# Optimization experiments

Hardware: AMD Instinct MI355X
Metric: run time of the kernel (lower is better)

The kernel has to match this reference:

```python
import jax, jax.numpy as jnp
import numpy as np

N_TOK = 131072
N_EMB = 1024
EMB_DIM = 64
COMMIT = 0.25


def setup_inputs() -> dict:
    key = jax.random.key(0)
    k1, k2 = jax.random.split(key)
    z_e = jax.random.normal(k1, (N_TOK, EMB_DIM), dtype=jnp.float32)
    # nn.init.uniform_(weight, -1/K, 1/K)
    codebook = jax.random.uniform(k2, (N_EMB, EMB_DIM), dtype=jnp.float32,
                                  minval=-1.0 / N_EMB, maxval=1.0 / N_EMB)
    return {"z_e": z_e, "codebook": codebook}


def reference(z_e, codebook):
    sg = jax.lax.stop_gradient
    # ||a-b||^2 = ||a||^2 + ||b||^2 - 2 a.b  (avoids [N,K,D] broadcast)
    d = (jnp.sum(z_e * z_e, axis=-1, keepdims=True)          # [N,1]
         + jnp.sum(codebook * codebook, axis=-1)[None, :]    # [1,K]
         - 2.0 * jnp.einsum('nd,kd->nk', z_e, codebook))     # [N,K]
    indices = jnp.argmin(d, axis=-1)                          # [N] int
    z_q = codebook[indices]                                   # [N,D] gather

    codebook_loss = jnp.mean((z_q - sg(z_e)) ** 2)
    commitment_loss = jnp.mean((z_e - sg(z_q)) ** 2)
    loss = codebook_loss + COMMIT * commitment_loss

    z_q_st = z_e + sg(z_q - z_e)                              # straight-through

    # avg_probs = one_hot(indices).mean(0) via scatter-add histogram
    counts = jnp.zeros((N_EMB,), dtype=jnp.float32).at[indices].add(1.0)
    avg_probs = counts / z_e.shape[0]
    perplexity = jnp.exp(-jnp.sum(avg_probs * jnp.log(avg_probs + 1e-10)))

    return z_q_st, loss, perplexity, indices
```

## Files before the change

kernel.cpp:

```cpp
#include <hip/hip_runtime.h>
#include <math.h>

#define NTOK 131072
#define NEMB 1024
#define DIM  64
#define OUT_LOSS (NTOK * DIM)
#define OUT_PERP (OUT_LOSS + 1)
#define OUT_IDX  (OUT_LOSS + 2)

#define EPS_FLAG 6e-5f

typedef short bf16x8 __attribute__((ext_vector_type(8)));
typedef float f32x4  __attribute__((ext_vector_type(4)));
typedef const __attribute__((address_space(1))) void* gas_t;
typedef __attribute__((address_space(3))) void* las_t;

__device__ __forceinline__ float sqb(float x) {
    float y = x * x;
    asm volatile("" : "+v"(y));
    return y;
}
#define NP_PAIRWISE_SQ64(GET, RES)                                     \
    do {                                                               \
        float r0 = sqb(GET(0)), r1 = sqb(GET(1)), r2 = sqb(GET(2)),    \
              r3 = sqb(GET(3)), r4 = sqb(GET(4)), r5 = sqb(GET(5)),    \
              r6 = sqb(GET(6)), r7 = sqb(GET(7));                      \
        _Pragma("unroll")                                              \
        for (int i = 8; i < 64; i += 8) {                              \
            r0 += sqb(GET(i + 0)); r1 += sqb(GET(i + 1));              \
            r2 += sqb(GET(i + 2)); r3 += sqb(GET(i + 3));              \
            r4 += sqb(GET(i + 4)); r5 += sqb(GET(i + 5));              \
            r6 += sqb(GET(i + 6)); r7 += sqb(GET(i + 7));              \
        }                                                              \
        RES = ((r0 + r1) + (r2 + r3)) + ((r4 + r5) + (r6 + r7));       \
    } while (0)

__device__ __forceinline__ unsigned short f2bf_rne(float x) {
    unsigned u = __float_as_uint(x);
    u += 0x7FFFu + ((u >> 16) & 1u);
    return (unsigned short)(u >> 16);
}
__device__ __forceinline__ float bf2f(unsigned short b) {
    return __uint_as_float(((unsigned)b) << 16);
}


__global__ void vq_prep(const float* __restrict__ cb, float* __restrict__ h,
                        unsigned short* __restrict__ ch, unsigned short* __restrict__ cl,
                        double* __restrict__ sse, int* __restrict__ counts,
                        int* __restrict__ done) {
    if (blockIdx.x == 0) {
        if (threadIdx.x == 0) { *sse = 0.0; *done = 0; }
        for (int i = threadIdx.x; i < NEMB * 16; i += 256) counts[i] = 0;
    }
    int k = blockIdx.x * 256 + threadIdx.x;
    if (k >= NEMB) return;
    float c[64];
    const float4* p = (const float4*)(cb + k * DIM);
#pragma unroll
    for (int q = 0; q < 16; ++q) {
        float4 v = p[q];
        c[4 * q] = v.x; c[4 * q + 1] = v.y; c[4 * q + 2] = v.z; c[4 * q + 3] = v.w;
    }
    float hk;
#define GETC(d) (c[d])
    NP_PAIRWISE_SQ64(GETC, hk);
#undef GETC
    h[k] = hk;
#pragma unroll
    for (int b = 0; b < 8; ++b) {
        unsigned uhv[4], ulv[4];
#pragma unroll
        for (int e = 0; e < 4; ++e) {
            float x0 = -2.0f * c[b * 8 + e * 2 + 0];
            float x1 = -2.0f * c[b * 8 + e * 2 + 1];
            unsigned short h0 = f2bf_rne(x0), h1 = f2bf_rne(x1);
            unsigned short l0 = f2bf_rne(x0 - bf2f(h0)), l1 = f2bf_rne(x1 - bf2f(h1));
            uhv[e] = (unsigned)h0 | ((unsigned)h1 << 16);
            ulv[e] = (unsigned)l0 | ((unsigned)l1 << 16);
        }
        *(uint4*)(ch + k * 64 + b * 8) = make_uint4(uhv[0], uhv[1], uhv[2], uhv[3]);
        *(uint4*)(cl + k * 64 + b * 8) = make_uint4(ulv[0], ulv[1], ulv[2], ulv[3]);
    }
}

__global__ __launch_bounds__(512) void vq_screen(
    const float*          __restrict__ ze,
    const float*          __restrict__ cb,
    const unsigned short* __restrict__ ch_g,
    const unsigned short* __restrict__ cl_g,
    const float*          __restrict__ h_g,
    float*                __restrict__ out,
    double*               __restrict__ sse_g,
    int*                  __restrict__ counts) {
    __shared__ __align__(16) char lds[53376];
    const int tid  = threadIdx.x;
    const int lane = tid & 63;
    const int wid  = tid >> 6;
    const int col  = lane & 15;
    const int grp  = lane >> 4;
    const int tbase = blockIdx.x * 256 + wid * 32;

    const int srow = tid >> 3, scol = tid & 7;
    const int srcoff = (srow * 8 + (scol ^ (srow & 7))) * 16;

    bf16x8 zh[2][2], zl[2][2];
#pragma unroll
    for (int tt = 0; tt < 2; ++tt)
#pragma unroll
        for (int s = 0; s < 2; ++s) {
            const float* zp = ze + (size_t)(tbase + tt * 16 + col) * 64 + s * 32 + grp * 8;
            float4 v0 = *(const float4*)(zp);
            float4 v1 = *(const float4*)(zp + 4);
            float zv[8] = {v0.x, v0.y, v0.z, v0.w, v1.x, v1.y, v1.z, v1.w};
            bf16x8 hfr, lfr;
#pragma unroll
            for (int j = 0; j < 8; ++j) {
                unsigned short hb = f2bf_rne(zv[j]);
                unsigned short lb = f2bf_rne(zv[j] - bf2f(hb));
                hfr[j] = (short)hb;
                lfr[j] = (short)lb;
            }
            zh[tt][s] = hfr;
            zl[tt][s] = lfr;
        }

    float m1[2] = {INFINITY, INFINITY}, m2[2] = {INFINITY, INFINITY};
    int   ki[2] = {0, 0};

#define STAGE(cc, b)                                                           \
    do {                                                                       \
        __builtin_amdgcn_global_load_lds(                                      \
            (gas_t)((const char*)ch_g + (cc) * 8192 + srcoff),                 \
            (las_t)(lds + (b) * 16384 + wid * 1024), 16, 0, 0);                \
        __builtin_amdgcn_global_load_lds(                                      \
            (gas_t)((const char*)cl_g + (cc) * 8192 + srcoff),                 \
            (las_t)(lds + (b) * 16384 + 8192 + wid * 1024), 16, 0, 0);         \
    } while (0)

#define COMPUTE(cc, b)                                                         \
    do {                                                                       \
        _Pragma("unroll")                                                      \
        for (int ct = 0; ct < 4; ++ct) {                                       \
            const int arow = (b) * 16384 + ct * 2048 + col * 128;              \
            bf16x8 ach0 = *(const bf16x8*)(lds + arow + ((((0 * 4) + grp) ^ (col & 7)) << 4)); \
            bf16x8 ach1 = *(const bf16x8*)(lds + arow + ((((1 * 4) + grp) ^ (col & 7)) << 4)); \
            bf16x8 acl0 = *(const bf16x8*)(lds + arow + 8192 + ((((0 * 4) + grp) ^ (col & 7)) << 4)); \
            bf16x8 acl1 = *(const bf16x8*)(lds + arow + 8192 + ((((1 * 4) + grp) ^ (col & 7)) << 4)); \
            f32x4 hv = *(const f32x4*)(lds + 49152 + (cc) * 256 + ct * 64 + grp * 16); \
            f32x4 acc0 = hv, acc1 = hv;                                        \
            acc0 = __builtin_amdgcn_mfma_f32_16x16x32_bf16(ach0, zh[0][0], acc0, 0, 0, 0); \
            acc1 = __builtin_amdgcn_mfma_f32_16x16x32_bf16(ach0, zh[1][0], acc1, 0, 0, 0); \
            acc0 = __builtin_amdgcn_mfma_f32_16x16x32_bf16(ach1, zh[0][1], acc0, 0, 0, 0); \
            acc1 = __builtin_amdgcn_mfma_f32_16x16x32_bf16(ach1, zh[1][1], acc1, 0, 0, 0); \
            acc0 = __builtin_amdgcn_mfma_f32_16x16x32_bf16(ach0, zl[0][0], acc0, 0, 0, 0); \
            acc1 = __builtin_amdgcn_mfma_f32_16x16x32_bf16(ach0, zl[1][0], acc1, 0, 0, 0); \
            acc0 = __builtin_amdgcn_mfma_f32_16x16x32_bf16(ach1, zl[0][1], acc0, 0, 0, 0); \
            acc1 = __builtin_amdgcn_mfma_f32_16x16x32_bf16(ach1, zl[1][1], acc1, 0, 0, 0); \
            acc0 = __builtin_amdgcn_mfma_f32_16x16x32_bf16(acl0, zh[0][0], acc0, 0, 0, 0); \
            acc1 = __builtin_amdgcn_mfma_f32_16x16x32_bf16(acl0, zh[1][0], acc1, 0, 0, 0); \
            acc0 = __builtin_amdgcn_mfma_f32_16x16x32_bf16(acl1, zh[0][1], acc0, 0, 0, 0); \
            acc1 = __builtin_amdgcn_mfma_f32_16x16x32_bf16(acl1, zh[1][1], acc1, 0, 0, 0); \
            const int kb = (cc) * 64 + ct * 16 + grp * 4;                      \
            _Pragma("unroll")                                                  \
            for (int j = 0; j < 4; ++j) {                                      \
                float s0 = acc0[j], s1 = acc1[j];                              \
                bool lt0 = s0 < m1[0], lt1 = s1 < m1[1];                       \
                m2[0] = fminf(m2[0], fmaxf(s0, m1[0]));                        \
                m2[1] = fminf(m2[1], fmaxf(s1, m1[1]));                        \
                ki[0] = lt0 ? (kb + j) : ki[0];                                \
                ki[1] = lt1 ? (kb + j) : ki[1];                                \
                m1[0] = fminf(m1[0], s0);                                      \
                m1[1] = fminf(m1[1], s1);                                      \
            }                                                                  \
        }                                                                      \
    } while (0)

#define CHUNK(cc, W)                                                           \
    do {                                                                       \
        asm volatile("s_waitcnt vmcnt(" #W ")" ::: "memory");                  \
        __builtin_amdgcn_s_barrier();                                          \
        __builtin_amdgcn_sched_barrier(0);                                     \
        if ((cc) + 2 < 16) STAGE((cc) + 2, ((cc) + 2) % 3);                    \
        COMPUTE(cc, (cc) % 3);                                                 \
    } while (0)

    __builtin_amdgcn_global_load_lds((gas_t)(h_g + tid),
                                     (las_t)(lds + 49152 + wid * 256), 4, 0, 0);
    __builtin_amdgcn_global_load_lds((gas_t)(h_g + 512 + tid),
                                     (las_t)(lds + 49152 + 2048 + wid * 256), 4, 0, 0);
    STAGE(0, 0);
    STAGE(1, 1);

    CHUNK(0, 2);  CHUNK(1, 2);  CHUNK(2, 2);  CHUNK(3, 2);
    CHUNK(4, 2);  CHUNK(5, 2);  CHUNK(6, 2);  CHUNK(7, 2);
    CHUNK(8, 2);  CHUNK(9, 2);  CHUNK(10, 2); CHUNK(11, 2);
    CHUNK(12, 2); CHUNK(13, 2); CHUNK(14, 2); CHUNK(15, 0);

#pragma unroll
    for (int d = 16; d <= 32; d <<= 1) {
#pragma unroll
        for (int tt = 0; tt < 2; ++tt) {
            float om1 = __shfl_xor(m1[tt], d, 64);
            float om2 = __shfl_xor(m2[tt], d, 64);
            int   oki = __shfl_xor(ki[tt], d, 64);
            m2[tt] = fminf(fminf(m2[tt], om2), fmaxf(m1[tt], om1));
            ki[tt] = (om1 < m1[tt]) ? oki : ki[tt];
            m1[tt] = fminf(m1[tt], om1);
        }
    }
    unsigned flagpack = ((m2[0] - m1[0] < EPS_FLAG) ? 1u : 0u)
                      | ((m2[1] - m1[1] < EPS_FLAG) ? 2u : 0u);
    if (lane < 16) {
#pragma unroll
        for (int tt = 0; tt < 2; ++tt) {
            int t = tbase + tt * 16 + lane;
            bool flag = (flagpack >> tt) & 1u;
            out[OUT_IDX + t] = flag ? -(float)(ki[tt] + 1) : (float)ki[tt];
        }
    }

    double lsse = 0.0;
    const int d4 = lane & 15;
#pragma unroll
    for (int iter = 0; iter < 8; ++iter) {
        const int j   = iter * 4 + grp;
        const int tt  = iter >> 2;
        const int src = j & 15;
        int k = __shfl(ki[tt], src, 64);
        unsigned fp = __shfl(flagpack, src, 64);
        if (!((fp >> tt) & 1u)) {
            const int t = tbase + j;
            float4 q  = *(const float4*)(cb + k * DIM + d4 * 4);
            float4 zv = *(const float4*)(ze + (size_t)t * DIM + d4 * 4);
            *(float4*)(out + (size_t)t * DIM + d4 * 4) = q;
            double dx = (double)q.x - (double)zv.x;
            double dy = (double)q.y - (double)zv.y;
            double dz = (double)q.z - (double)zv.z;
            double dw = (double)q.w - (double)zv.w;
            lsse = fma(dx, dx, lsse); lsse = fma(dy, dy, lsse);
            lsse = fma(dz, dz, lsse); lsse = fma(dw, dw, lsse);
            if (d4 == 0) atomicAdd(&counts[k * 16], 1);
        }
    }
#pragma unroll
    for (int off = 32; off > 0; off >>= 1)
        lsse += __shfl_down(lsse, off, 64);
    double* red = (double*)(lds + 53312);
    if (lane == 0) red[wid] = lsse;
    __syncthreads();
    if (tid == 0) {
        double bs = ((red[0] + red[1]) + (red[2] + red[3]))
                  + ((red[4] + red[5]) + (red[6] + red[7]));
        atomicAdd(sse_g, bs);
    }
}

__global__ __launch_bounds__(512) void vq_rescue(
    const float* __restrict__ ze, const float* __restrict__ cb,
    const float* __restrict__ h_g, float* __restrict__ out,
    double* __restrict__ sse_g, int* __restrict__ counts,
    int* __restrict__ done) {
    __shared__ __align__(16) float4 cbl[512 * 17];
    __shared__ float zst[8][64];
    __shared__ unsigned long long keys[8][64];
    __shared__ float hl[NEMB];
    __shared__ int loc[512];
    __shared__ int nloc;
    __shared__ double red[8];
    __shared__ int flagS;
    const int tid  = threadIdx.x;
    const int lane = tid & 63;
    const int wid  = tid >> 6;
    const int tbase = blockIdx.x * 512;

    if (tid == 0) nloc = 0;
    for (int i = tid; i < NEMB; i += 512) hl[i] = h_g[i];
    __syncthreads();
    float fidx = out[OUT_IDX + tbase + tid];
    if (fidx < 0.0f) { int s = atomicAdd(&nloc, 1); loc[s] = tid; }
    __syncthreads();
    const int nq = nloc;
    double lsse = 0.0;

    if (nq > 0) {
        const float4* cb4 = (const float4*)cb;
        for (int hf = 0; hf < 2; ++hf) {
            __syncthreads();
#pragma unroll
            for (int j = 0; j < 16; ++j) {
                int f = tid + j * 512;
                int code = f >> 4, d4 = f & 15;
                cbl[code * 17 + d4] = cb4[(size_t)(hf * 512 + code) * 16 + d4];
            }
            __syncthreads();

            for (int i = wid; i < nq; i += 8) {
                const int t = tbase + loc[i];
                const int slot = i >> 3;

                zst[wid][lane] = ze[(size_t)t * 64 + lane];
                __builtin_amdgcn_wave_barrier();
                asm volatile("s_waitcnt lgkmcnt(0)" ::: "memory");
                __builtin_amdgcn_sched_barrier(0);

                float sz;
#define GZ(d) (zst[wid][d])
                NP_PAIRWISE_SQ64(GZ, sz);
#undef GZ

                float acc[8] = {0.f, 0.f, 0.f, 0.f, 0.f, 0.f, 0.f, 0.f};
                const float4* zr4 = (const float4*)zst[wid];
#pragma unroll
                for (int d4 = 0; d4 < 16; ++d4) {
                    float4 zq = zr4[d4];
#pragma unroll
                    for (int cc = 0; cc < 8; ++cc) {
                        float4 cv = cbl[(lane + 64 * cc) * 17 + d4];
                        acc[cc] = fmaf(cv.x, zq.x, acc[cc]);
                        acc[cc] = fmaf(cv.y, zq.y, acc[cc]);
                        acc[cc] = fmaf(cv.z, zq.z, acc[cc]);
                        acc[cc] = fmaf(cv.w, zq.w, acc[cc]);
                    }
                }
                unsigned long long key = ~0ull;
#pragma unroll
                for (int cc = 0; cc < 8; ++cc) {
                    unsigned k = (unsigned)(hf * 512 + lane + 64 * cc);
                    float dk = (sz + hl[k]) - 2.0f * acc[cc];
                    unsigned long long c =
                        ((unsigned long long)__float_as_uint(dk) << 32) | k;
                    key = c < key ? c : key;
                }
#pragma unroll
                for (int dd = 1; dd < 64; dd <<= 1) {
                    unsigned long long o = __shfl_xor(key, dd, 64);
                    key = o < key ? o : key;
                }
                if (hf == 0) {
                    if (lane == 0) keys[wid][slot] = key;
                } else {
                    unsigned long long k0 = keys[wid][slot];
                    if (k0 < key) key = k0;
                    int newk = (int)(unsigned)(key & 0xFFFFFFFFull);
                    float q  = cb[newk * 64 + lane];
                    float zv = zst[wid][lane];
                    out[(size_t)t * 64 + lane] = q;
                    double diff = (double)q - (double)zv;
                    lsse = fma(diff, diff, lsse);
                    if (lane == 0) {
                        out[OUT_IDX + t] = (float)newk;
                        atomicAdd(&counts[newk * 16], 1);
                    }
                }
            }
        }
    }

#pragma unroll
    for (int off = 32; off > 0; off >>= 1)
        lsse += __shfl_down(lsse, off, 64);
    if (lane == 0) red[wid] = lsse;
    __syncthreads();
    if (tid == 0) {
        double bs = ((red[0] + red[1]) + (red[2] + red[3]))
                  + ((red[4] + red[5]) + (red[6] + red[7]));
        if (bs != 0.0) atomicAdd(sse_g, bs);
        __threadfence();
        flagS = (atomicAdd(done, 1) == 255);
    }
    __syncthreads();

    if (flagS) {
        __threadfence();
        double* red2 = (double*)cbl;
        double local = 0.0;
        for (int k = tid; k < NEMB; k += 512) {
            int cv = __hip_atomic_load(&counts[k * 16], __ATOMIC_RELAXED, __HIP_MEMORY_SCOPE_AGENT);
            double p = (double)cv / (double)NTOK;
            local += p * log(p + 1e-10);
        }
        red2[tid] = local;
        __syncthreads();
        for (int s = 256; s > 0; s >>= 1) {
            if (tid < s) red2[tid] += red2[tid + s];
            __syncthreads();
        }
        if (tid == 0) {
            double sv = __hip_atomic_load(sse_g, __ATOMIC_RELAXED, __HIP_MEMORY_SCOPE_AGENT);
            double mse = sv / ((double)NTOK * (double)DIM);
            out[OUT_LOSS] = (float)(1.25 * mse);
            out[OUT_PERP] = (float)exp(-red2[0]);
        }
    }
}

extern "C" void kernel_launch(void* const* d_in, const int* in_sizes, int n_in,
                              void* d_out, int out_size, void* d_ws, size_t ws_size,
                              hipStream_t stream) {
    const float* ze = (const float*)d_in[0];
    const float* cb = (const float*)d_in[1];
    float* out = (float*)d_out;

    char* w = (char*)d_ws;
    double*         sse    = (double*)w;
    int*            counts = (int*)(w + 64);
    int*            done   = (int*)(w + 65600);
    float*          h      = (float*)(w + 65664);
    unsigned short* ch     = (unsigned short*)(w + 69760);
    unsigned short* cl     = (unsigned short*)(w + 200832);

    vq_prep<<<NEMB / 256, 256, 0, stream>>>(cb, h, ch, cl, sse, counts, done);
    vq_screen<<<NTOK / 256, 512, 0, stream>>>(ze, cb, ch, cl, h, out, sse, counts);
    vq_rescue<<<NTOK / 512, 512, 0, stream>>>(ze, cb, h, out, sse, counts, done);
}
```

Before: 125.6 us.

## Double tokens per wave in screen kernel to amortize codebook LDS reads

Each wave now handles 64 tokens (four 16-token tiles) instead of 32, so every codebook fragment read from LDS feeds twice as many MFMAs. The grid is halved and the block keeps 512 threads. The MFMA chain is also restructured per tile into one dependent accumulator chain of six MFMAs. The tt index in the epilogue changes from iter>>2 to j>>4, which is equivalent to the old mapping. This raises register pressure (more z fragments and min state), adds a launch_bounds min-blocks hint, and reduces the number of blocks to 256, which may underfill the GPU. Each 6-MFMA chain per tile is serial, which may expose MFMA latency.

Result: slower. 157.0 us (+25.0%).

```diff
diff --git a/kernel.cpp b/kernel.cpp
--- a/kernel.cpp
+++ b/kernel.cpp
@@ -84,7 +84,7 @@
     }
 }
 
-__global__ __launch_bounds__(512) void vq_screen(
+__global__ __launch_bounds__(512, 4) void vq_screen(
     const float*          __restrict__ ze,
     const float*          __restrict__ cb,
     const unsigned short* __restrict__ ch_g,
@@ -99,14 +99,14 @@
     const int wid  = tid >> 6;
     const int col  = lane & 15;
     const int grp  = lane >> 4;
-    const int tbase = blockIdx.x * 256 + wid * 32;
+    const int tbase = blockIdx.x * 512 + wid * 64;
 
     const int srow = tid >> 3, scol = tid & 7;
     const int srcoff = (srow * 8 + (scol ^ (srow & 7))) * 16;
 
-    bf16x8 zh[2][2], zl[2][2];
-#pragma unroll
-    for (int tt = 0; tt < 2; ++tt)
+    bf16x8 zh[4][2], zl[4][2];
+#pragma unroll
+    for (int tt = 0; tt < 4; ++tt)
 #pragma unroll
         for (int s = 0; s < 2; ++s) {
             const float* zp = ze + (size_t)(tbase + tt * 16 + col) * 64 + s * 32 + grp * 8;
@@ -125,8 +125,9 @@
             zl[tt][s] = lfr;
         }
 
-    float m1[2] = {INFINITY, INFINITY}, m2[2] = {INFINITY, INFINITY};
-    int   ki[2] = {0, 0};
+    float m1[4] = {INFINITY, INFINITY, INFINITY, INFINITY};
+    float m2[4] = {INFINITY, INFINITY, INFINITY, INFINITY};
+    int   ki[4] = {0, 0, 0, 0};
 
 #define STAGE(cc, b)                                                           \
     do {                                                                       \
@@ -148,30 +149,23 @@
             bf16x8 acl0 = *(const bf16x8*)(lds + arow + 8192 + ((((0 * 4) + grp) ^ (col & 7)) << 4)); \
             bf16x8 acl1 = *(const bf16x8*)(lds + arow + 8192 + ((((1 * 4) + grp) ^ (col & 7)) << 4)); \
             f32x4 hv = *(const f32x4*)(lds + 49152 + (cc) * 256 + ct * 64 + grp * 16); \
-            f32x4 acc0 = hv, acc1 = hv;                                        \
-            acc0 = __builtin_amdgcn_mfma_f32_16x16x32_bf16(ach0, zh[0][0], acc0, 0, 0, 0); \
-            acc1 = __builtin_amdgcn_mfma_f32_16x16x32_bf16(ach0, zh[1][0], acc1, 0, 0, 0); \
-            acc0 = __builtin_amdgcn_mfma_f32_16x16x32_bf16(ach1, zh[0][1], acc0, 0, 0, 0); \
-            acc1 = __builtin_amdgcn_mfma_f32_16x16x32_bf16(ach1, zh[1][1], acc1, 0, 0, 0); \
-            acc0 = __builtin_amdgcn_mfma_f32_16x16x32_bf16(ach0, zl[0][0], acc0, 0, 0, 0); \
-            acc1 = __builtin_amdgcn_mfma_f32_16x16x32_bf16(ach0, zl[1][0], acc1, 0, 0, 0); \
-            acc0 = __builtin_amdgcn_mfma_f32_16x16x32_bf16(ach1, zl[0][1], acc0, 0, 0, 0); \
-            acc1 = __builtin_amdgcn_mfma_f32_16x16x32_bf16(ach1, zl[1][1], acc1, 0, 0, 0); \
-            acc0 = __builtin_amdgcn_mfma_f32_16x16x32_bf16(acl0, zh[0][0], acc0, 0, 0, 0); \
-            acc1 = __builtin_amdgcn_mfma_f32_16x16x32_bf16(acl0, zh[1][0], acc1, 0, 0, 0); \
-            acc0 = __builtin_amdgcn_mfma_f32_16x16x32_bf16(acl1, zh[0][1], acc0, 0, 0, 0); \
-            acc1 = __builtin_amdgcn_mfma_f32_16x16x32_bf16(acl1, zh[1][1], acc1, 0, 0, 0); \
             const int kb = (cc) * 64 + ct * 16 + grp * 4;                      \
             _Pragma("unroll")                                                  \
-            for (int j = 0; j < 4; ++j) {                                      \
-                float s0 = acc0[j], s1 = acc1[j];                              \
-                bool lt0 = s0 < m1[0], lt1 = s1 < m1[1];                       \
-                m2[0] = fminf(m2[0], fmaxf(s0, m1[0]));                        \
-                m2[1] = fminf(m2[1], fmaxf(s1, m1[1]));                        \
-                ki[0] = lt0 ? (kb + j) : ki[0];                                \
-                ki[1] = lt1 ? (kb + j) : ki[1];                                \
-                m1[0] = fminf(m1[0], s0);                                      \
-                m1[1] = fminf(m1[1], s1);                                      \
+            for (int tt = 0; tt < 4; ++tt) {                                   \
+                f32x4 acc = hv;                                                \
+                acc = __builtin_amdgcn_mfma_f32_16x16x32_bf16(ach0, zh[tt][0], acc, 0, 0, 0); \
+                acc = __builtin_amdgcn_mfma_f32_16x16x32_bf16(ach1, zh[tt][1], acc, 0, 0, 0); \
+                acc = __builtin_amdgcn_mfma_f32_16x16x32_bf16(ach0, zl[tt][0], acc, 0, 0, 0); \
+                acc = __builtin_amdgcn_mfma_f32_16x16x32_bf16(ach1, zl[tt][1], acc, 0, 0, 0); \
+                acc = __builtin_amdgcn_mfma_f32_16x16x32_bf16(acl0, zh[tt][0], acc, 0, 0, 0); \
+                acc = __builtin_amdgcn_mfma_f32_16x16x32_bf16(acl1, zh[tt][1], acc, 0, 0, 0); \
+                _Pragma("unroll")                                              \
+                for (int j = 0; j < 4; ++j) {                                  \
+                    float s = acc[j];                                          \
+                    m2[tt] = fminf(m2[tt], fmaxf(s, m1[tt]));                  \
+                    ki[tt] = (s < m1[tt]) ? (kb + j) : ki[tt];                 \
+                    m1[tt] = fminf(m1[tt], s);                                 \
+                }                                                              \
             }                                                                  \
         }                                                                      \
     } while (0)
@@ -200,7 +194,7 @@
 #pragma unroll
     for (int d = 16; d <= 32; d <<= 1) {
 #pragma unroll
-        for (int tt = 0; tt < 2; ++tt) {
+        for (int tt = 0; tt < 4; ++tt) {
             float om1 = __shfl_xor(m1[tt], d, 64);
             float om2 = __shfl_xor(m2[tt], d, 64);
             int   oki = __shfl_xor(ki[tt], d, 64);
@@ -210,10 +204,12 @@
         }
     }
     unsigned flagpack = ((m2[0] - m1[0] < EPS_FLAG) ? 1u : 0u)
-                      | ((m2[1] - m1[1] < EPS_FLAG) ? 2u : 0u);
+                      | ((m2[1] - m1[1] < EPS_FLAG) ? 2u : 0u)
+                      | ((m2[2] - m1[2] < EPS_FLAG) ? 4u : 0u)
+                      | ((m2[3] - m1[3] < EPS_FLAG) ? 8u : 0u);
     if (lane < 16) {
 #pragma unroll
-        for (int tt = 0; tt < 2; ++tt) {
+        for (int tt = 0; tt < 4; ++tt) {
             int t = tbase + tt * 16 + lane;
             bool flag = (flagpack >> tt) & 1u;
             out[OUT_IDX + t] = flag ? -(float)(ki[tt] + 1) : (float)ki[tt];
@@ -223,9 +219,9 @@
     double lsse = 0.0;
     const int d4 = lane & 15;
 #pragma unroll
-    for (int iter = 0; iter < 8; ++iter) {
+    for (int iter = 0; iter < 16; ++iter) {
         const int j   = iter * 4 + grp;
-        const int tt  = iter >> 2;
+        const int tt  = j >> 4;
         const int src = j & 15;
         int k = __shfl(ki[tt], src, 64);
         unsigned fp = __shfl(flagpack, src, 64);
@@ -411,6 +407,6 @@
     unsigned short* cl     = (unsigned short*)(w + 200832);
 
     vq_prep<<<NEMB / 256, 256, 0, stream>>>(cb, h, ch, cl, sse, counts, done);
-    vq_screen<<<NTOK / 256, 512, 0, stream>>>(ze, cb, ch, cl, h, out, sse, counts);
+    vq_screen<<<NTOK / 512, 512, 0, stream>>>(ze, cb, ch, cl, h, out, sse, counts);
     vq_rescue<<<NTOK / 512, 512, 0, stream>>>(ze, cb, h, out, sse, counts, done);
 }
```

## Track top-3 candidates in screen so rescue checks only two codes

Applied to the files above, without the earlier changes.

The screening kernel now keeps the best three distances per token instead of two. For flagged near-tie tokens it writes the runner-up index to an aux buffer, plus a bit saying whether the third candidate is also within the tie margin. The rescue kernel then does exact fp32 distances only against the top two codes for most flagged tokens, falling back to a full 1024-code scan only for 'deep' ties. This removes the large shared-memory codebook staging and full scans in rescue, at the cost of more compare/select work in the screen's hot loop and a correctness reliance on the third-best bound.

Measured after the change: 133.7 us. 1.06x slower.

```diff
diff --git a/kernel.cpp b/kernel.cpp
--- a/kernel.cpp
+++ b/kernel.cpp
@@ -91,6 +91,7 @@
     const unsigned short* __restrict__ cl_g,
     const float*          __restrict__ h_g,
     float*                __restrict__ out,
+    int*                  __restrict__ aux,
     double*               __restrict__ sse_g,
     int*                  __restrict__ counts) {
     __shared__ __align__(16) char lds[53376];
@@ -126,7 +127,8 @@
         }
 
     float m1[2] = {INFINITY, INFINITY}, m2[2] = {INFINITY, INFINITY};
-    int   ki[2] = {0, 0};
+    float m3[2] = {INFINITY, INFINITY};
+    int   ki[2] = {0, 0}, i2[2] = {0, 0};
 
 #define STAGE(cc, b)                                                           \
     do {                                                                       \
@@ -136,6 +138,16 @@
         __builtin_amdgcn_global_load_lds(                                      \
             (gas_t)((const char*)cl_g + (cc) * 8192 + srcoff),                 \
             (las_t)(lds + (b) * 16384 + 8192 + wid * 1024), 16, 0, 0);         \
+    } while (0)
+
+#define TOP3UPD(tt, s, kk)                                                     \
+    do {                                                                       \
+        bool lt1 = (s) < m1[tt], lt2 = (s) < m2[tt], lt3 = (s) < m3[tt];       \
+        m3[tt] = lt2 ? m2[tt] : (lt3 ? (s) : m3[tt]);                          \
+        i2[tt] = lt1 ? ki[tt] : (lt2 ? (kk) : i2[tt]);                         \
+        m2[tt] = lt1 ? m1[tt] : (lt2 ? (s) : m2[tt]);                          \
+        ki[tt] = lt1 ? (kk) : ki[tt];                                          \
+        m1[tt] = lt1 ? (s) : m1[tt];                                           \
     } while (0)
 
 #define COMPUTE(cc, b)                                                         \
@@ -164,14 +176,8 @@
             const int kb = (cc) * 64 + ct * 16 + grp * 4;                      \
             _Pragma("unroll")                                                  \
             for (int j = 0; j < 4; ++j) {                                      \
-                float s0 = acc0[j], s1 = acc1[j];                              \
-                bool lt0 = s0 < m1[0], lt1 = s1 < m1[1];                       \
-                m2[0] = fminf(m2[0], fmaxf(s0, m1[0]));                        \
-                m2[1] = fminf(m2[1], fmaxf(s1, m1[1]));                        \
-                ki[0] = lt0 ? (kb + j) : ki[0];                                \
-                ki[1] = lt1 ? (kb + j) : ki[1];                                \
-                m1[0] = fminf(m1[0], s0);                                      \
-                m1[1] = fminf(m1[1], s1);                                      \
+                TOP3UPD(0, acc0[j], kb + j);                                   \
+                TOP3UPD(1, acc1[j], kb + j);                                   \
             }                                                                  \
         }                                                                      \
     } while (0)
@@ -201,22 +207,42 @@
     for (int d = 16; d <= 32; d <<= 1) {
 #pragma unroll
         for (int tt = 0; tt < 2; ++tt) {
-            float om1 = __shfl_xor(m1[tt], d, 64);
-            float om2 = __shfl_xor(m2[tt], d, 64);
-            int   oki = __shfl_xor(ki[tt], d, 64);
-            m2[tt] = fminf(fminf(m2[tt], om2), fmaxf(m1[tt], om1));
-            ki[tt] = (om1 < m1[tt]) ? oki : ki[tt];
-            m1[tt] = fminf(m1[tt], om1);
+            float b1 = __shfl_xor(m1[tt], d, 64);
+            float b2 = __shfl_xor(m2[tt], d, 64);
+            float b3 = __shfl_xor(m3[tt], d, 64);
+            int  jb1 = __shfl_xor(ki[tt], d, 64);
+            int  jb2 = __shfl_xor(i2[tt], d, 64);
+            bool sw  = b1 < m1[tt];
+            float hi = sw ? m1[tt] : b1;
+            int  jhi = sw ? ki[tt] : jb1;
+            float c1 = sw ? b1 : m1[tt];
+            int   j1 = sw ? jb1 : ki[tt];
+            float mn2 = fminf(m2[tt], b2);
+            int   jm2 = (m2[tt] <= b2) ? i2[tt] : jb2;
+            float c2  = fminf(hi, mn2);
+            int   j2  = (hi <= mn2) ? jhi : jm2;
+            float mid = fmaxf(fminf(hi, m2[tt]),
+                              fminf(fmaxf(hi, m2[tt]), b2));
+            float c3  = fminf(mid, fminf(m3[tt], b3));
+            m1[tt] = c1; ki[tt] = j1; m2[tt] = c2; i2[tt] = j2; m3[tt] = c3;
         }
     }
     unsigned flagpack = ((m2[0] - m1[0] < EPS_FLAG) ? 1u : 0u)
                       | ((m2[1] - m1[1] < EPS_FLAG) ? 2u : 0u);
+    unsigned deeppack = ((m3[0] - m1[0] < EPS_FLAG) ? 1u : 0u)
+                      | ((m3[1] - m1[1] < EPS_FLAG) ? 2u : 0u);
     if (lane < 16) {
 #pragma unroll
         for (int tt = 0; tt < 2; ++tt) {
             int t = tbase + tt * 16 + lane;
             bool flag = (flagpack >> tt) & 1u;
-            out[OUT_IDX + t] = flag ? -(float)(ki[tt] + 1) : (float)ki[tt];
+            if (flag) {
+                out[OUT_IDX + t] = -(float)(ki[tt] + 1);
+                aux[t] = (int)((unsigned)i2[tt]
+                               | (((deeppack >> tt) & 1u) << 31));
+            } else {
+                out[OUT_IDX + t] = (float)ki[tt];
+            }
         }
     }
 
@@ -258,101 +284,123 @@
 
 __global__ __launch_bounds__(512) void vq_rescue(
     const float* __restrict__ ze, const float* __restrict__ cb,
-    const float* __restrict__ h_g, float* __restrict__ out,
-    double* __restrict__ sse_g, int* __restrict__ counts,
-    int* __restrict__ done) {
-    __shared__ __align__(16) float4 cbl[512 * 17];
+    const float* __restrict__ h_g, const int* __restrict__ aux,
+    float* __restrict__ out, double* __restrict__ sse_g,
+    int* __restrict__ counts, int* __restrict__ done) {
+    __shared__ int loc[512];
+    __shared__ int kfin[512];
+    __shared__ int dlist[512];
+    __shared__ int nloc, ndeep;
     __shared__ float zst[8][64];
-    __shared__ unsigned long long keys[8][64];
-    __shared__ float hl[NEMB];
-    __shared__ int loc[512];
-    __shared__ int nloc;
-    __shared__ double red[8];
+    __shared__ double red2[512];
     __shared__ int flagS;
     const int tid  = threadIdx.x;
     const int lane = tid & 63;
     const int wid  = tid >> 6;
     const int tbase = blockIdx.x * 512;
 
-    if (tid == 0) nloc = 0;
-    for (int i = tid; i < NEMB; i += 512) hl[i] = h_g[i];
+    if (tid == 0) { nloc = 0; ndeep = 0; }
     __syncthreads();
-    float fidx = out[OUT_IDX + tbase + tid];
-    if (fidx < 0.0f) { int s = atomicAdd(&nloc, 1); loc[s] = tid; }
+    {
+        float fidx = out[OUT_IDX + tbase + tid];
+        if (fidx < 0.0f) { int s = atomicAdd(&nloc, 1); loc[s] = tid; }
+    }
     __syncthreads();
     const int nq = nloc;
     double lsse = 0.0;
 
     if (nq > 0) {
-        const float4* cb4 = (const float4*)cb;
-        for (int hf = 0; hf < 2; ++hf) {
-            __syncthreads();
-#pragma unroll
-            for (int j = 0; j < 16; ++j) {
-                int f = tid + j * 512;
-                int code = f >> 4, d4 = f & 15;
-                cbl[code * 17 + d4] = cb4[(size_t)(hf * 512 + code) * 16 + d4];
-            }
-            __syncthreads();
-
-            for (int i = wid; i < nq; i += 8) {
-                const int t = tbase + loc[i];
-                const int slot = i >> 3;
-
-                zst[wid][lane] = ze[(size_t)t * 64 + lane];
-                __builtin_amdgcn_wave_barrier();
-                asm volatile("s_waitcnt lgkmcnt(0)" ::: "memory");
-                __builtin_amdgcn_sched_barrier(0);
-
-                float sz;
+        const int e = lane * 8 + wid;
+        if (e < nq) {
+            const int t = tbase + loc[e];
+            const int i1 = (int)(-out[OUT_IDX + t]) - 1;
+            const unsigned a = (unsigned)aux[t];
+            if (a >> 31) {
+                int s = atomicAdd(&ndeep, 1);
+                dlist[s] = e;
+            } else {
+                const int i2v = (int)(a & 1023u);
+                const float4* zp  = (const float4*)(ze + (size_t)t * 64);
+                const float4* c1p = (const float4*)(cb + i1 * 64);
+                const float4* c2p = (const float4*)(cb + i2v * 64);
+                float r0 = 0, r1 = 0, r2 = 0, r3 = 0, r4 = 0, r5 = 0, r6 = 0, r7 = 0;
+                float A1 = 0.f, A2 = 0.f;
+#pragma unroll
+                for (int q = 0; q < 16; ++q) {
+                    float4 zv = zp[q], cv1 = c1p[q], cv2 = c2p[q];
+                    if (q & 1) {
+                        r4 += sqb(zv.x); r5 += sqb(zv.y);
+                        r6 += sqb(zv.z); r7 += sqb(zv.w);
+                    } else {
+                        r0 += sqb(zv.x); r1 += sqb(zv.y);
+                        r2 += sqb(zv.z); r3 += sqb(zv.w);
+                    }
+                    A1 = fmaf(cv1.x, zv.x, A1); A1 = fmaf(cv1.y, zv.y, A1);
+                    A1 = fmaf(cv1.z, zv.z, A1); A1 = fmaf(cv1.w, zv.w, A1);
+                    A2 = fmaf(cv2.x, zv.x, A2); A2 = fmaf(cv2.y, zv.y, A2);
+                    A2 = fmaf(cv2.z, zv.z, A2); A2 = fmaf(cv2.w, zv.w, A2);
+                }
+                float sz = ((r0 + r1) + (r2 + r3)) + ((r4 + r5) + (r6 + r7));
+                float d1 = (sz + h_g[i1])  - 2.0f * A1;
+                float d2 = (sz + h_g[i2v]) - 2.0f * A2;
+                unsigned long long k1 =
+                    ((unsigned long long)__float_as_uint(d1) << 32) | (unsigned)i1;
+                unsigned long long k2 =
+                    ((unsigned long long)__float_as_uint(d2) << 32) | (unsigned)i2v;
+                kfin[e] = (int)(unsigned)((k1 < k2 ? k1 : k2) & 0xFFFFFFFFull);
+            }
+        }
+        __syncthreads();
+
+        for (int i = wid; i < ndeep; i += 8) {
+            const int e2 = dlist[i];
+            const int t = tbase + loc[e2];
+            zst[wid][lane] = ze[(size_t)t * 64 + lane];
+            __builtin_amdgcn_wave_barrier();
+            asm volatile("s_waitcnt lgkmcnt(0)" ::: "memory");
+            __builtin_amdgcn_sched_barrier(0);
+            float sz;
 #define GZ(d) (zst[wid][d])
-                NP_PAIRWISE_SQ64(GZ, sz);
+            NP_PAIRWISE_SQ64(GZ, sz);
 #undef GZ
-
-                float acc[8] = {0.f, 0.f, 0.f, 0.f, 0.f, 0.f, 0.f, 0.f};
-                const float4* zr4 = (const float4*)zst[wid];
-#pragma unroll
-                for (int d4 = 0; d4 < 16; ++d4) {
-                    float4 zq = zr4[d4];
-#pragma unroll
-                    for (int cc = 0; cc < 8; ++cc) {
-                        float4 cv = cbl[(lane + 64 * cc) * 17 + d4];
-                        acc[cc] = fmaf(cv.x, zq.x, acc[cc]);
-                        acc[cc] = fmaf(cv.y, zq.y, acc[cc]);
-                        acc[cc] = fmaf(cv.z, zq.z, acc[cc]);
-                        acc[cc] = fmaf(cv.w, zq.w, acc[cc]);
-                    }
+            const float4* cb4 = (const float4*)cb;
+            const float4* zr4 = (const float4*)zst[wid];
+            unsigned long long key = ~0ull;
+            for (int cc = 0; cc < 16; ++cc) {
+                const int code = lane + 64 * cc;
+                float acc = 0.f;
+#pragma unroll
+                for (int d4i = 0; d4i < 16; ++d4i) {
+                    float4 zq = zr4[d4i];
+                    float4 cv = cb4[(size_t)code * 16 + d4i];
+                    acc = fmaf(cv.x, zq.x, acc); acc = fmaf(cv.y, zq.y, acc);
+                    acc = fmaf(cv.z, zq.z, acc); acc = fmaf(cv.w, zq.w, acc);
                 }
-                unsigned long long key = ~0ull;
-#pragma unroll
-                for (int cc = 0; cc < 8; ++cc) {
-                    unsigned k = (unsigned)(hf * 512 + lane + 64 * cc);
-                    float dk = (sz + hl[k]) - 2.0f * acc[cc];
-                    unsigned long long c =
-                        ((unsigned long long)__float_as_uint(dk) << 32) | k;
-                    key = c < key ? c : key;
-                }
-#pragma unroll
-                for (int dd = 1; dd < 64; dd <<= 1) {
-                    unsigned long long o = __shfl_xor(key, dd, 64);
-                    key = o < key ? o : key;
-                }
-                if (hf == 0) {
-                    if (lane == 0) keys[wid][slot] = key;
-                } else {
-                    unsigned long long k0 = keys[wid][slot];
-                    if (k0 < key) key = k0;
-                    int newk = (int)(unsigned)(key & 0xFFFFFFFFull);
-                    float q  = cb[newk * 64 + lane];
-                    float zv = zst[wid][lane];
-                    out[(size_t)t * 64 + lane] = q;
-                    double diff = (double)q - (double)zv;
-                    lsse = fma(diff, diff, lsse);
-                    if (lane == 0) {
-                        out[OUT_IDX + t] = (float)newk;
-                        atomicAdd(&counts[newk * 16], 1);
-                    }
-                }
+                float dk = (sz + h_g[code]) - 2.0f * acc;
+                unsigned long long c =
+                    ((unsigned long long)__float_as_uint(dk) << 32) | (unsigned)code;
+                key = c < key ? c : key;
+            }
+#pragma unroll
+            for (int dd = 1; dd < 64; dd <<= 1) {
+                unsigned long long o = __shfl_xor(key, dd, 64);
+                key = o < key ? o : key;
+            }
+            if (lane == 0) kfin[e2] = (int)(unsigned)(key & 0xFFFFFFFFull);
+        }
+        __syncthreads();
+
+        for (int e3 = wid; e3 < nq; e3 += 8) {
+            const int k = kfin[e3];
+            const int t = tbase + loc[e3];
+            float q  = cb[k * 64 + lane];
+            float zv = ze[(size_t)t * 64 + lane];
+            out[(size_t)t * 64 + lane] = q;
+            double diff = (double)q - (double)zv;
+            lsse = fma(diff, diff, lsse);
+            if (lane == 0) {
+                out[OUT_IDX + t] = (float)k;
+                atomicAdd(&counts[k * 16], 1);
             }
         }
     }
@@ -360,11 +408,11 @@
 #pragma unroll
     for (int off = 32; off > 0; off >>= 1)
         lsse += __shfl_down(lsse, off, 64);
-    if (lane == 0) red[wid] = lsse;
+    if (lane == 0) red2[wid] = lsse;
     __syncthreads();
     if (tid == 0) {
-        double bs = ((red[0] + red[1]) + (red[2] + red[3]))
-                  + ((red[4] + red[5]) + (red[6] + red[7]));
+        double bs = ((red2[0] + red2[1]) + (red2[2] + red2[3]))
+                  + ((red2[4] + red2[5]) + (red2[6] + red2[7]));
         if (bs != 0.0) atomicAdd(sse_g, bs);
         __threadfence();
         flagS = (atomicAdd(done, 1) == 255);
@@ -373,7 +421,6 @@
 
     if (flagS) {
         __threadfence();
-        double* red2 = (double*)cbl;
         double local = 0.0;
         for (int k = tid; k < NEMB; k += 512) {
             int cv = __hip_atomic_load(&counts[k * 16], __ATOMIC_RELAXED, __HIP_MEMORY_SCOPE_AGENT);
@@ -409,8 +456,9 @@
     float*          h      = (float*)(w + 65664);
     unsigned short* ch     = (unsigned short*)(w + 69760);
     unsigned short* cl     = (unsigned short*)(w + 200832);
+    int*            aux    = (int*)(w + 331904);
 
     vq_prep<<<NEMB / 256, 256, 0, stream>>>(cb, h, ch, cl, sse, counts, done);
-    vq_screen<<<NTOK / 256, 512, 0, stream>>>(ze, cb, ch, cl, h, out, sse, counts);
-    vq_rescue<<<NTOK / 512, 512, 0, stream>>>(ze, cb, h, out, sse, counts, done);
-}
+    vq_screen<<<NTOK / 256, 512, 0, stream>>>(ze, cb, ch, cl, h, out, aux, sse, counts);
+    vq_rescue<<<NTOK / 512, 512, 0, stream>>>(ze, cb, h, aux, out, sse, counts, done);
+}
```
